# Optimization experiments

Measured on AMD Instinct MI355X. Metric: run time of the kernel, lower is better.

Reference implementation:

```python
import jax, jax.numpy as jnp
import numpy as np

SCALE = 1.0

def setup_inputs() -> dict:
    key = jax.random.key(0)
    k1, k2, k3 = jax.random.split(key, 3)
    N, K, H, W = 4, 8, 512, 512
    C, P = 16, 1000000
    fragments = jax.random.randint(k1, (N, K, H, W), 0, P, dtype=jnp.int32)
    zbuf = jax.random.uniform(k2, (N, K, H, W), dtype=jnp.float32)
    ptclds = jax.random.normal(k3, (C, P), dtype=jnp.float32)
    return {"fragments": fragments, "zbuf": zbuf, "ptclds": ptclds}

def reference(fragments, zbuf, ptclds):
    # zbuf < 0 means no point assigned; replace with -1e-4 as in original
    z = jnp.where(zbuf < 0, jnp.float32(-0.0001), zbuf)
    importance = 1.0 / (z + 1e-06)                      # (N, K, H, W)
    weights = jax.nn.softmax(importance * SCALE, axis=1)  # softmax over K
    # gather point features: (C, N, K, H, W)
    gathered = ptclds[:, fragments]
    # weighted sum over K -> (N, C, H, W)
    images = jnp.einsum('nkhw,cnkhw->nchw', weights, gathered)
    return images
```

## Files before the change

kernel.cpp:

```cpp
#include <hip/hip_runtime.h>

#define NN 4
#define KK 8
#define HH 512
#define WW 512
#define CC 16
#define PP 1000000

__global__ __launch_bounds__(256) void transpose_tbl(
    const float* __restrict__ ptclds, float* __restrict__ tbl) {
  __shared__ float lds[64][17];
  const int base = blockIdx.x * 64;
  const int p  = threadIdx.x & 63;
  const int c0 = (threadIdx.x >> 6) * 4;
#pragma unroll
  for (int i = 0; i < 4; ++i) {
    int c = c0 + i;
    lds[p][c] = ptclds[(size_t)c * PP + base + p];
  }
  __syncthreads();
  const int po = threadIdx.x >> 2;
  const int q  = threadIdx.x & 3;
  float4 v = make_float4(lds[po][q * 4 + 0], lds[po][q * 4 + 1],
                         lds[po][q * 4 + 2], lds[po][q * 4 + 3]);
  reinterpret_cast<float4*>(tbl)[(size_t)blockIdx.x * 256 + threadIdx.x] = v;
}

template <int TRANSPOSED>
__global__ __launch_bounds__(256) void composite(
    const int* __restrict__ frag, const float* __restrict__ zbuf,
    const float* __restrict__ tbl, float* __restrict__ out) {
  const int HW = HH * WW;
  int g = blockIdx.x * blockDim.x + threadIdx.x;
  if (g >= NN * HW) return;
  int n = g >> 18;
  int hw = g & (HW - 1);

  const int* fp = frag + (size_t)n * KK * HW + hw;
  const float* zp = zbuf + (size_t)n * KK * HW + hw;

  int idx[KK];
  float e[KK];
  float m = -3.402823e38f;
#pragma unroll
  for (int k = 0; k < KK; ++k) {
    float z = zp[k * HW];
    idx[k] = fp[k * HW];
    z = (z < 0.0f) ? -0.0001f : z;
    float im = 1.0f / (z + 1e-6f);
    e[k] = im;
    m = fmaxf(m, im);
  }
  float s = 0.0f;
#pragma unroll
  for (int k = 0; k < KK; ++k) {
    e[k] = __expf(e[k] - m);
    s += e[k];
  }
  float rs = 1.0f / s;

  float acc[CC];
#pragma unroll
  for (int c = 0; c < CC; ++c) acc[c] = 0.0f;

  if (TRANSPOSED) {
#pragma unroll
    for (int kb = 0; kb < 2; ++kb) {
      float4 q0[4], q1[4], q2[4], q3[4];
#pragma unroll
      for (int j = 0; j < 4; ++j) {
        const float4* tp =
            reinterpret_cast<const float4*>(tbl + (size_t)idx[kb * 4 + j] * CC);
        q0[j] = tp[0]; q1[j] = tp[1]; q2[j] = tp[2]; q3[j] = tp[3];
      }
#pragma unroll
      for (int j = 0; j < 4; ++j) {
        float wk = e[kb * 4 + j];
        acc[0]  += wk * q0[j].x;  acc[1]  += wk * q0[j].y;
        acc[2]  += wk * q0[j].z;  acc[3]  += wk * q0[j].w;
        acc[4]  += wk * q1[j].x;  acc[5]  += wk * q1[j].y;
        acc[6]  += wk * q1[j].z;  acc[7]  += wk * q1[j].w;
        acc[8]  += wk * q2[j].x;  acc[9]  += wk * q2[j].y;
        acc[10] += wk * q2[j].z;  acc[11] += wk * q2[j].w;
        acc[12] += wk * q3[j].x;  acc[13] += wk * q3[j].y;
        acc[14] += wk * q3[j].z;  acc[15] += wk * q3[j].w;
      }
    }
  } else {
#pragma unroll
    for (int k = 0; k < KK; ++k) {
#pragma unroll
      for (int c = 0; c < CC; ++c)
        acc[c] += e[k] * tbl[(size_t)c * PP + idx[k]];
    }
  }

  float* op = out + (size_t)n * CC * HW + hw;
#pragma unroll
  for (int c = 0; c < CC; ++c) op[c * HW] = acc[c] * rs;
}

extern "C" void kernel_launch(void* const* d_in, const int* in_sizes, int n_in,
                              void* d_out, int out_size, void* d_ws, size_t ws_size,
                              hipStream_t stream) {
  const int* frag = (const int*)d_in[0];
  const float* zbuf = (const float*)d_in[1];
  const float* ptclds = (const float*)d_in[2];
  float* out = (float*)d_out;

  const int HW = HH * WW;
  const int npix = NN * HW;
  const size_t tbl_bytes = (size_t)PP * CC * sizeof(float);

  if (ws_size >= tbl_bytes) {
    float* tbl = (float*)d_ws;
    transpose_tbl<<<PP / 64, 256, 0, stream>>>(ptclds, tbl);
    composite<1><<<(npix + 255) / 256, 256, 0, stream>>>(frag, zbuf, tbl, out);
  } else {
    composite<0><<<(npix + 255) / 256, 256, 0, stream>>>(frag, zbuf, ptclds, out);
  }
}
```

Measured before the change: 322.4 us.

## Issue all gathers early, use nontemporal streaming loads/stores, widen transpose blocks

The transpose kernel now handles 256 points per block and reads ptclds with float4 nontemporal loads. The composite kernel issues all eight 64-byte table gathers before the softmax math, separated by a sched_barrier, so gather latency overlaps with the exp work. Fragment, zbuf and output traffic use nontemporal loads and stores, which should keep the streamed data from evicting the gather table out of cache. Occupancy is hinted via launch_bounds(256,2), and the per-pixel bounds check is dropped. Holding 32 float4 registers for the gathers per thread raises register pressure, which may reduce occupancy.

```diff
diff --git a/kernel.cpp b/kernel.cpp
--- a/kernel.cpp
+++ b/kernel.cpp
@@ -6,98 +6,145 @@
 #define WW 512
 #define CC 16
 #define PP 1000000
+#define HWPIX (HH * WW)
+
+typedef float f32x4 __attribute__((ext_vector_type(4)));
 
 __global__ __launch_bounds__(256) void transpose_tbl(
     const float* __restrict__ ptclds, float* __restrict__ tbl) {
-  __shared__ float lds[64][17];
-  const int base = blockIdx.x * 64;
-  const int p  = threadIdx.x & 63;
-  const int c0 = (threadIdx.x >> 6) * 4;
+  __shared__ float lds[256][17];
+  const int base = blockIdx.x * 256;
+  const int c = threadIdx.x >> 4;
+  const int t = threadIdx.x & 15;
 #pragma unroll
-  for (int i = 0; i < 4; ++i) {
-    int c = c0 + i;
-    lds[p][c] = ptclds[(size_t)c * PP + base + p];
+  for (int r = 0; r < 4; ++r) {
+    int p = r * 64 + t * 4;
+    int pg = base + p;
+    if (pg < PP) {
+      f32x4 v = __builtin_nontemporal_load(
+          reinterpret_cast<const f32x4*>(ptclds + (size_t)c * PP + pg));
+      lds[p + 0][c] = v.x;
+      lds[p + 1][c] = v.y;
+      lds[p + 2][c] = v.z;
+      lds[p + 3][c] = v.w;
+    }
   }
   __syncthreads();
-  const int po = threadIdx.x >> 2;
-  const int q  = threadIdx.x & 3;
-  float4 v = make_float4(lds[po][q * 4 + 0], lds[po][q * 4 + 1],
-                         lds[po][q * 4 + 2], lds[po][q * 4 + 3]);
-  reinterpret_cast<float4*>(tbl)[(size_t)blockIdx.x * 256 + threadIdx.x] = v;
+  const int q = threadIdx.x & 3;
+#pragma unroll
+  for (int w = 0; w < 4; ++w) {
+    int po = (threadIdx.x >> 2) + 64 * w;
+    int pg = base + po;
+    if (pg < PP) {
+      f32x4 v;
+      v.x = lds[po][q * 4 + 0];
+      v.y = lds[po][q * 4 + 1];
+      v.z = lds[po][q * 4 + 2];
+      v.w = lds[po][q * 4 + 3];
+      reinterpret_cast<f32x4*>(tbl)[(size_t)pg * 4 + q] = v;
+    }
+  }
 }
 
 template <int TRANSPOSED>
-__global__ __launch_bounds__(256) void composite(
+__global__ __launch_bounds__(256, 2) void composite(
     const int* __restrict__ frag, const float* __restrict__ zbuf,
     const float* __restrict__ tbl, float* __restrict__ out) {
-  const int HW = HH * WW;
-  int g = blockIdx.x * blockDim.x + threadIdx.x;
-  if (g >= NN * HW) return;
+  int g = blockIdx.x * 256 + threadIdx.x;
   int n = g >> 18;
-  int hw = g & (HW - 1);
+  int hw = g & (HWPIX - 1);
 
-  const int* fp = frag + (size_t)n * KK * HW + hw;
-  const float* zp = zbuf + (size_t)n * KK * HW + hw;
+  const int* fp = frag + (size_t)n * KK * HWPIX + hw;
+  const float* zp = zbuf + (size_t)n * KK * HWPIX + hw;
 
   int idx[KK];
-  float e[KK];
-  float m = -3.402823e38f;
 #pragma unroll
-  for (int k = 0; k < KK; ++k) {
-    float z = zp[k * HW];
-    idx[k] = fp[k * HW];
-    z = (z < 0.0f) ? -0.0001f : z;
-    float im = 1.0f / (z + 1e-6f);
-    e[k] = im;
-    m = fmaxf(m, im);
-  }
-  float s = 0.0f;
+  for (int k = 0; k < KK; ++k)
+    idx[k] = __builtin_nontemporal_load(fp + k * HWPIX);
+  float zv[KK];
 #pragma unroll
-  for (int k = 0; k < KK; ++k) {
-    e[k] = __expf(e[k] - m);
-    s += e[k];
-  }
-  float rs = 1.0f / s;
+  for (int k = 0; k < KK; ++k)
+    zv[k] = __builtin_nontemporal_load(zp + k * HWPIX);
 
   float acc[CC];
-#pragma unroll
-  for (int c = 0; c < CC; ++c) acc[c] = 0.0f;
+  float s;
 
   if (TRANSPOSED) {
+    f32x4 q[KK][4];
 #pragma unroll
-    for (int kb = 0; kb < 2; ++kb) {
-      float4 q0[4], q1[4], q2[4], q3[4];
+    for (int k = 0; k < KK; ++k) {
+      const f32x4* tp = reinterpret_cast<const f32x4*>(tbl) + (size_t)idx[k] * 4;
+      q[k][0] = tp[0];
+      q[k][1] = tp[1];
+      q[k][2] = tp[2];
+      q[k][3] = tp[3];
+    }
+    float e[KK];
+    float m = -3.402823e38f;
 #pragma unroll
-      for (int j = 0; j < 4; ++j) {
-        const float4* tp =
-            reinterpret_cast<const float4*>(tbl + (size_t)idx[kb * 4 + j] * CC);
-        q0[j] = tp[0]; q1[j] = tp[1]; q2[j] = tp[2]; q3[j] = tp[3];
-      }
+    for (int k = 0; k < KK; ++k) {
+      float z = zv[k];
+      z = (z < 0.0f) ? -0.0001f : z;
+      float im = 1.0f / (z + 1e-6f);
+      e[k] = im;
+      m = fmaxf(m, im);
+    }
+    s = 0.0f;
 #pragma unroll
-      for (int j = 0; j < 4; ++j) {
-        float wk = e[kb * 4 + j];
-        acc[0]  += wk * q0[j].x;  acc[1]  += wk * q0[j].y;
-        acc[2]  += wk * q0[j].z;  acc[3]  += wk * q0[j].w;
-        acc[4]  += wk * q1[j].x;  acc[5]  += wk * q1[j].y;
-        acc[6]  += wk * q1[j].z;  acc[7]  += wk * q1[j].w;
-        acc[8]  += wk * q2[j].x;  acc[9]  += wk * q2[j].y;
-        acc[10] += wk * q2[j].z;  acc[11] += wk * q2[j].w;
-        acc[12] += wk * q3[j].x;  acc[13] += wk * q3[j].y;
-        acc[14] += wk * q3[j].z;  acc[15] += wk * q3[j].w;
+    for (int k = 0; k < KK; ++k) {
+      e[k] = __expf(e[k] - m);
+      s += e[k];
+    }
+    __builtin_amdgcn_sched_barrier(0);
+#pragma unroll
+    for (int k = 0; k < KK; ++k) {
+      float wk = e[k];
+#pragma unroll
+      for (int c4 = 0; c4 < 4; ++c4) {
+        if (k == 0) {
+          acc[c4 * 4 + 0] = wk * q[k][c4].x;
+          acc[c4 * 4 + 1] = wk * q[k][c4].y;
+          acc[c4 * 4 + 2] = wk * q[k][c4].z;
+          acc[c4 * 4 + 3] = wk * q[k][c4].w;
+        } else {
+          acc[c4 * 4 + 0] += wk * q[k][c4].x;
+          acc[c4 * 4 + 1] += wk * q[k][c4].y;
+          acc[c4 * 4 + 2] += wk * q[k][c4].z;
+          acc[c4 * 4 + 3] += wk * q[k][c4].w;
+        }
       }
     }
   } else {
+    float e[KK];
+    float m = -3.402823e38f;
 #pragma unroll
     for (int k = 0; k < KK; ++k) {
+      float z = zv[k];
+      z = (z < 0.0f) ? -0.0001f : z;
+      float im = 1.0f / (z + 1e-6f);
+      e[k] = im;
+      m = fmaxf(m, im);
+    }
+    s = 0.0f;
+#pragma unroll
+    for (int k = 0; k < KK; ++k) {
+      e[k] = __expf(e[k] - m);
+      s += e[k];
+    }
+#pragma unroll
+    for (int c = 0; c < CC; ++c) acc[c] = 0.0f;
+#pragma unroll
+    for (int k = 0; k < KK; ++k)
 #pragma unroll
       for (int c = 0; c < CC; ++c)
         acc[c] += e[k] * tbl[(size_t)c * PP + idx[k]];
-    }
   }
 
-  float* op = out + (size_t)n * CC * HW + hw;
+  float rs = 1.0f / s;
+  float* op = out + (size_t)n * CC * HWPIX + hw;
 #pragma unroll
-  for (int c = 0; c < CC; ++c) op[c * HW] = acc[c] * rs;
+  for (int c = 0; c < CC; ++c)
+    __builtin_nontemporal_store(acc[c] * rs, op + c * HWPIX);
 }
 
 extern "C" void kernel_launch(void* const* d_in, const int* in_sizes, int n_in,
@@ -108,15 +155,14 @@
   const float* ptclds = (const float*)d_in[2];
   float* out = (float*)d_out;
 
-  const int HW = HH * WW;
-  const int npix = NN * HW;
+  const int npix = NN * HWPIX;
   const size_t tbl_bytes = (size_t)PP * CC * sizeof(float);
 
   if (ws_size >= tbl_bytes) {
     float* tbl = (float*)d_ws;
-    transpose_tbl<<<PP / 64, 256, 0, stream>>>(ptclds, tbl);
-    composite<1><<<(npix + 255) / 256, 256, 0, stream>>>(frag, zbuf, tbl, out);
+    transpose_tbl<<<(PP + 255) / 256, 256, 0, stream>>>(ptclds, tbl);
+    composite<1><<<npix / 256, 256, 0, stream>>>(frag, zbuf, tbl, out);
   } else {
-    composite<0><<<(npix + 255) / 256, 256, 0, stream>>>(frag, zbuf, ptclds, out);
+    composite<0><<<npix / 256, 256, 0, stream>>>(frag, zbuf, ptclds, out);
   }
 }
```

After: 308.0 us. 4.5% less time.
